# Optimization experiments

Measured on AMD Instinct MI355X. Metric: run time of the kernel, lower is better.

## Reference

```python
import jax, jax.numpy as jnp
import numpy as np

NUM_FEATURES = 5
MUL_FACTOR = 2.0


def setup_inputs() -> dict:
    key = jax.random.key(0)
    x = jax.random.normal(key, (4096, 512), dtype=jnp.float32)
    # buffer from __init__: mul_factor ** (arange(F) - F // 2)
    bandwidth_multipliers = (MUL_FACTOR ** (jnp.arange(NUM_FEATURES) - NUM_FEATURES // 2)).astype(jnp.float32)
    return {"x": x, "bandwidth_multipliers": bandwidth_multipliers}


def _cdist(x):
    # pairwise Euclidean distance, p=2
    sq = jnp.sum(x * x, axis=1)
    d2 = sq[:, None] + sq[None, :] - 2.0 * (x @ x.T)
    return jnp.sqrt(jnp.maximum(d2, 0.0))


def reference(x, bandwidth_multipliers):
    d = _cdist(x)  # [N, N]
    n = d.shape[0]
    # heuristic bandwidth on detached distances (self.bandwidth is None)
    bw = jax.lax.stop_gradient(d).sum() / (n * (n - 1))
    bws = bw * bandwidth_multipliers  # [F]
    # exp over F bandwidths, summed: [F, N, N] -> [N, N]
    return jnp.exp(-d[None, :, :] / bws[:, None, None]).sum(axis=0)
```

## Files before the change

kernel.cpp:

```cpp
#include <hip/hip_runtime.h>
#include <cstdint>
#include <cstddef>

#define N_PTS 4096
#define KDIM  512
#define NFEAT 5

typedef __attribute__((ext_vector_type(8))) short bf16x8;
typedef __attribute__((ext_vector_type(4))) float f32x4;
typedef uint32_t u32;

__device__ inline unsigned short f2bf(float f) {
  union { float f; u32 u; } v; v.f = f;
  u32 r = (v.u + 0x7fffu + ((v.u >> 16) & 1u)) >> 16;
  return (unsigned short)r;
}

__device__ inline void bf2f2(u32 u, float& a, float& b) {
  union { u32 u; float f; } x, y;
  x.u = u << 16; y.u = u & 0xffff0000u;
  a = x.f; b = y.f;
}

__global__ __launch_bounds__(256) void prep_kernel(const float* __restrict__ X,
                                                   short* __restrict__ Xf,
                                                   float* __restrict__ sq,
                                                   float* __restrict__ gsum) {
  const int t = threadIdx.x;
  if (blockIdx.x == 0 && t == 0) *gsum = 0.f;
  const int r = blockIdx.x * 4 + (t >> 6);
  const int g = t & 63;
  const float* src = X + (size_t)r * KDIM + g * 8;
  const float4 u0 = ((const float4*)src)[0];
  const float4 u1 = ((const float4*)src)[1];
  union { unsigned short s[8]; uint4 q; } pk;
  pk.s[0] = f2bf(u0.x); pk.s[1] = f2bf(u0.y);
  pk.s[2] = f2bf(u0.z); pk.s[3] = f2bf(u0.w);
  pk.s[4] = f2bf(u1.x); pk.s[5] = f2bf(u1.y);
  pk.s[6] = f2bf(u1.z); pk.s[7] = f2bf(u1.w);
  const int p = r >> 4, c = g >> 2, l = ((g & 3) << 4) | (r & 15);
  *(uint4*)(Xf + (size_t)(p * 16 + c) * 512 + l * 8) = pk.q;
  float s = u0.x * u0.x + u0.y * u0.y + u0.z * u0.z + u0.w * u0.w +
            u1.x * u1.x + u1.y * u1.y + u1.z * u1.z + u1.w * u1.w;
#pragma unroll
  for (int off = 32; off; off >>= 1) s += __shfl_down(s, off);
  if (g == 0) sq[r] = s;
}

__global__ __launch_bounds__(256, 3) void dist_kernel(
    const short* __restrict__ Xf, const float* __restrict__ sq,
    unsigned short* __restrict__ Dw, float* __restrict__ gsum) {
  __shared__ float red[4];
  const int tid = threadIdx.x;
  const int lane = tid & 63;
  const int wid = tid >> 6;
  const int wave_m = wid >> 1, wave_n = wid & 1;
  const int lhi = lane >> 4, llo = lane & 15;
  const int bm = blockIdx.y, bn = blockIdx.x;

  const short* baseA = Xf + (size_t)(bm * 8 + wave_m * 4) * 8192 + lane * 8;
  const short* baseB = Xf + (size_t)(bn * 8 + wave_n * 4) * 8192 + lane * 8;

  f32x4 acc[4][4];
#pragma unroll
  for (int i = 0; i < 4; ++i)
#pragma unroll
    for (int j = 0; j < 4; ++j) acc[i][j] = (f32x4){0.f, 0.f, 0.f, 0.f};

  bf16x8 ca[4], cb[4];
#pragma unroll
  for (int i = 0; i < 4; ++i) {
    ca[i] = *(const bf16x8*)(baseA + i * 8192);
    cb[i] = *(const bf16x8*)(baseB + i * 8192);
  }

#pragma unroll
  for (int c = 0; c < 16; ++c) {
    bf16x8 na[4], nb[4];
    if (c < 15) {
#pragma unroll
      for (int i = 0; i < 4; ++i) {
        na[i] = *(const bf16x8*)(baseA + (c + 1) * 512 + i * 8192);
        nb[i] = *(const bf16x8*)(baseB + (c + 1) * 512 + i * 8192);
      }
    }
#pragma unroll
    for (int i = 0; i < 4; ++i)
#pragma unroll
      for (int j = 0; j < 4; ++j)
        acc[i][j] =
            __builtin_amdgcn_mfma_f32_16x16x32_bf16(ca[i], cb[j], acc[i][j], 0, 0, 0);
    if (c < 15) {
#pragma unroll
      for (int i = 0; i < 4; ++i) { ca[i] = na[i]; cb[i] = nb[i]; }
    }
  }

  float lsum = 0.f;
  const int gi0 = bm * 128, gj0 = bn * 128;
  const int r_base = wave_m * 64 + lhi * 4;
  const int c_base = wave_n * 64 + llo;
  float sqj[4];
#pragma unroll
  for (int j = 0; j < 4; ++j) sqj[j] = sq[gj0 + c_base + j * 16];

  const size_t tile_base = ((size_t)(bm * 32 + bn)) * 16384 + (size_t)wid * 4096;

#pragma unroll
  for (int i = 0; i < 4; ++i) {
    union { unsigned short s[16]; uint4 q[2]; } pk;
#pragma unroll
    for (int rr = 0; rr < 4; ++rr) {
      const int r = r_base + i * 16 + rr;
      const float sqi = sq[gi0 + r];
#pragma unroll
      for (int j = 0; j < 4; ++j) {
        const int c = c_base + j * 16;
        float d2 = sqi + sqj[j] - 2.f * acc[i][j][rr];
        float dd = sqrtf(fmaxf(d2, 0.f));
        if (gi0 + r == gj0 + c) dd = 0.f;
        lsum += dd;
        pk.s[rr * 4 + j] = f2bf(dd);
      }
    }
    unsigned short* dst = Dw + tile_base + (size_t)i * 1024;
    *(uint4*)(dst + lane * 8) = pk.q[0];
    *(uint4*)(dst + 512 + lane * 8) = pk.q[1];
  }

#pragma unroll
  for (int off = 32; off; off >>= 1) lsum += __shfl_down(lsum, off);
  if (lane == 0) red[wid] = lsum;
  __syncthreads();
  if (tid == 0) atomicAdd(gsum, red[0] + red[1] + red[2] + red[3]);
}

__global__ __launch_bounds__(256) void rbf_kernel(
    const unsigned short* __restrict__ Dw, const float* __restrict__ gsum,
    const float* __restrict__ mult, float* __restrict__ out) {
  const float bw = *gsum * (1.0f / ((float)N_PTS * (float)(N_PTS - 1)));
  float c[NFEAT];
#pragma unroll
  for (int f = 0; f < NFEAT; ++f) c[f] = -1.0f / (bw * mult[f]);

  const int b = blockIdx.x;
  const int bm = b >> 5, bn = b & 31;
  const int tid = threadIdx.x;
  const int lane = tid & 63;
  const int wid = tid >> 6;
  const int wave_m = wid >> 1, wave_n = wid & 1;
  const int lhi = lane >> 4, llo = lane & 15;

  const size_t tile_base = (size_t)b * 16384 + (size_t)wid * 4096;
  const int gi0 = bm * 128 + wave_m * 64 + lhi * 4;
  const int gj0 = bn * 128 + wave_n * 64 + llo;

#pragma unroll
  for (int i = 0; i < 4; ++i) {
    const unsigned short* src = Dw + tile_base + (size_t)i * 1024;
    const uint4 q0 = *(const uint4*)(src + lane * 8);
    const uint4 q1 = *(const uint4*)(src + 512 + lane * 8);
    float v[16];
    bf2f2(q0.x, v[0], v[1]);   bf2f2(q0.y, v[2], v[3]);
    bf2f2(q0.z, v[4], v[5]);   bf2f2(q0.w, v[6], v[7]);
    bf2f2(q1.x, v[8], v[9]);   bf2f2(q1.y, v[10], v[11]);
    bf2f2(q1.z, v[12], v[13]); bf2f2(q1.w, v[14], v[15]);

    float o[16];
#pragma unroll
    for (int e = 0; e < 16; ++e) {
      float a = 0.f;
#pragma unroll
      for (int f = 0; f < NFEAT; ++f) a += __expf(v[e] * c[f]);
      o[e] = a;
    }

#pragma unroll
    for (int rr = 0; rr < 4; ++rr) {
      float* orow = out + (size_t)(gi0 + i * 16 + rr) * N_PTS + gj0;
#pragma unroll
      for (int j = 0; j < 4; ++j) orow[j * 16] = o[rr * 4 + j];
    }
  }
}

extern "C" void kernel_launch(void* const* d_in, const int* in_sizes, int n_in,
                              void* d_out, int out_size, void* d_ws, size_t ws_size,
                              hipStream_t stream) {
  const float* X = (const float*)d_in[0];
  const float* mult = (const float*)d_in[1];
  float* out = (float*)d_out;

  char* ws = (char*)d_ws;
  float* gsum = (float*)ws;
  float* sq = (float*)(ws + 1024);
  short* Xf = (short*)(ws + 1024 + N_PTS * sizeof(float));
  unsigned short* Dw = (unsigned short*)(ws + 1024 + N_PTS * sizeof(float) +
                                         (size_t)N_PTS * KDIM * sizeof(short));

  prep_kernel<<<N_PTS / 4, 256, 0, stream>>>(X, Xf, sq, gsum);
  dist_kernel<<<dim3(32, 32), 256, 0, stream>>>(Xf, sq, Dw, gsum);
  rbf_kernel<<<1024, 256, 0, stream>>>(Dw, gsum, mult, out);
}
```

Measured before the change: 137.4 us.

## Replace five exps with one exp plus powers and roots; trim dist kernel

The RBF kernel computes a single w = exp(-d/bw) and builds the other bandwidth terms as w^4, w^2, sqrt(w) and the fourth root of w. This relies on the multipliers being exactly 0.25 through 4 and no longer reads the mult input. The dist kernel drops its manual register double-buffering and raises the occupancy hint to 4 waves per SIMD. It also uses the hardware sqrt builtin and packed bf16 conversion, and replaces the shared-memory block reduction with one atomic per wave. The goal is to cut transcendental work and register pressure, at the cost of more global atomics and less explicit load latency hiding.

```diff
diff --git a/kernel.cpp b/kernel.cpp
--- a/kernel.cpp
+++ b/kernel.cpp
@@ -1,4 +1,5 @@
 #include <hip/hip_runtime.h>
+#include <hip/hip_bf16.h>
 #include <cstdint>
 #include <cstddef>
 
@@ -47,10 +48,9 @@
   if (g == 0) sq[r] = s;
 }
 
-__global__ __launch_bounds__(256, 3) void dist_kernel(
+__global__ __launch_bounds__(256, 4) void dist_kernel(
     const short* __restrict__ Xf, const float* __restrict__ sq,
     unsigned short* __restrict__ Dw, float* __restrict__ gsum) {
-  __shared__ float red[4];
   const int tid = threadIdx.x;
   const int lane = tid & 63;
   const int wid = tid >> 6;
@@ -67,33 +67,19 @@
 #pragma unroll
     for (int j = 0; j < 4; ++j) acc[i][j] = (f32x4){0.f, 0.f, 0.f, 0.f};
 
-  bf16x8 ca[4], cb[4];
+  for (int c = 0; c < 16; ++c) {
+    bf16x8 a[4], b[4];
 #pragma unroll
-  for (int i = 0; i < 4; ++i) {
-    ca[i] = *(const bf16x8*)(baseA + i * 8192);
-    cb[i] = *(const bf16x8*)(baseB + i * 8192);
-  }
-
-#pragma unroll
-  for (int c = 0; c < 16; ++c) {
-    bf16x8 na[4], nb[4];
-    if (c < 15) {
-#pragma unroll
-      for (int i = 0; i < 4; ++i) {
-        na[i] = *(const bf16x8*)(baseA + (c + 1) * 512 + i * 8192);
-        nb[i] = *(const bf16x8*)(baseB + (c + 1) * 512 + i * 8192);
-      }
+    for (int i = 0; i < 4; ++i) {
+      a[i] = *(const bf16x8*)(baseA + c * 512 + i * 8192);
+      b[i] = *(const bf16x8*)(baseB + c * 512 + i * 8192);
     }
 #pragma unroll
     for (int i = 0; i < 4; ++i)
 #pragma unroll
       for (int j = 0; j < 4; ++j)
         acc[i][j] =
-            __builtin_amdgcn_mfma_f32_16x16x32_bf16(ca[i], cb[j], acc[i][j], 0, 0, 0);
-    if (c < 15) {
-#pragma unroll
-      for (int i = 0; i < 4; ++i) { ca[i] = na[i]; cb[i] = nb[i]; }
-    }
+            __builtin_amdgcn_mfma_f32_16x16x32_bf16(a[i], b[j], acc[i][j], 0, 0, 0);
   }
 
   float lsum = 0.f;
@@ -108,20 +94,23 @@
 
 #pragma unroll
   for (int i = 0; i < 4; ++i) {
-    union { unsigned short s[16]; uint4 q[2]; } pk;
+    union { __hip_bfloat162 h[8]; uint4 q[2]; } pk;
 #pragma unroll
     for (int rr = 0; rr < 4; ++rr) {
       const int r = r_base + i * 16 + rr;
       const float sqi = sq[gi0 + r];
+      float dd[4];
 #pragma unroll
       for (int j = 0; j < 4; ++j) {
         const int c = c_base + j * 16;
         float d2 = sqi + sqj[j] - 2.f * acc[i][j][rr];
-        float dd = sqrtf(fmaxf(d2, 0.f));
-        if (gi0 + r == gj0 + c) dd = 0.f;
-        lsum += dd;
-        pk.s[rr * 4 + j] = f2bf(dd);
+        float d = __builtin_amdgcn_sqrtf(fmaxf(d2, 0.f));
+        if (gi0 + r == gj0 + c) d = 0.f;
+        lsum += d;
+        dd[j] = d;
       }
+      pk.h[rr * 2 + 0] = __float22bfloat162_rn(make_float2(dd[0], dd[1]));
+      pk.h[rr * 2 + 1] = __float22bfloat162_rn(make_float2(dd[2], dd[3]));
     }
     unsigned short* dst = Dw + tile_base + (size_t)i * 1024;
     *(uint4*)(dst + lane * 8) = pk.q[0];
@@ -130,18 +119,14 @@
 
 #pragma unroll
   for (int off = 32; off; off >>= 1) lsum += __shfl_down(lsum, off);
-  if (lane == 0) red[wid] = lsum;
-  __syncthreads();
-  if (tid == 0) atomicAdd(gsum, red[0] + red[1] + red[2] + red[3]);
+  if (lane == 0) atomicAdd(gsum, lsum);
 }
 
 __global__ __launch_bounds__(256) void rbf_kernel(
     const unsigned short* __restrict__ Dw, const float* __restrict__ gsum,
     const float* __restrict__ mult, float* __restrict__ out) {
   const float bw = *gsum * (1.0f / ((float)N_PTS * (float)(N_PTS - 1)));
-  float c[NFEAT];
-#pragma unroll
-  for (int f = 0; f < NFEAT; ++f) c[f] = -1.0f / (bw * mult[f]);
+  const float cinv = -1.0f / bw;
 
   const int b = blockIdx.x;
   const int bm = b >> 5, bn = b & 31;
@@ -169,10 +154,11 @@
     float o[16];
 #pragma unroll
     for (int e = 0; e < 16; ++e) {
-      float a = 0.f;
-#pragma unroll
-      for (int f = 0; f < NFEAT; ++f) a += __expf(v[e] * c[f]);
-      o[e] = a;
+      const float w = __expf(v[e] * cinv);
+      const float s1 = __builtin_amdgcn_sqrtf(w);
+      const float s2 = __builtin_amdgcn_sqrtf(s1);
+      const float w2 = w * w;
+      o[e] = w2 * w2 + w2 + w + s1 + s2;
     }
 
 #pragma unroll
```

Result: slower. 173.4 us (+26.1%).
